# Kernel optimization log

Hardware: AMD Instinct MI355X
Metric: run time of the kernel (lower is better)

The kernel has to match this reference:

```python
import jax, jax.numpy as jnp
import numpy as np

B, S, DIM_IN = 2, 2048, 1024
H, DQ, DK = 16, 64, 64


def setup_inputs() -> dict:
    key = jax.random.key(0)
    ks = jax.random.split(key, 11)
    s_in = 1.0 / np.sqrt(DIM_IN)
    s_o = 1.0 / np.sqrt(H * DK)
    return {
        "Q": jax.random.normal(ks[0], (B, S, DIM_IN), jnp.float32),
        "K": jax.random.normal(ks[1], (B, S, DIM_IN), jnp.float32),
        "V": jax.random.normal(ks[2], (B, S, DIM_IN), jnp.float32),
        # per-head projection weights, stacked over heads: [H, dim_in, d]
        "Wq": jax.random.uniform(ks[3], (H, DIM_IN, DQ), jnp.float32, -s_in, s_in),
        "bq": jax.random.uniform(ks[4], (H, DQ), jnp.float32, -s_in, s_in),
        "Wk": jax.random.uniform(ks[5], (H, DIM_IN, DK), jnp.float32, -s_in, s_in),
        "bk": jax.random.uniform(ks[6], (H, DK), jnp.float32, -s_in, s_in),
        "Wv": jax.random.uniform(ks[7], (H, DIM_IN, DK), jnp.float32, -s_in, s_in),
        "bv": jax.random.uniform(ks[8], (H, DK), jnp.float32, -s_in, s_in),
        # output projection: Linear(H*DK, DIM_IN)
        "Wo": jax.random.uniform(ks[9], (H * DK, DIM_IN), jnp.float32, -s_o, s_o),
        "bo": jax.random.uniform(ks[10], (DIM_IN,), jnp.float32, -s_o, s_o),
    }


def reference(Q, K, V, Wq, bq, Wk, bk, Wv, bv, Wo, bo):
    # per-head linear projections: [B,S,din] x [H,din,d] -> [B,H,S,d]
    q = jnp.einsum("bsd,hdq->bhsq", Q, Wq) + bq[None, :, None, :]
    k = jnp.einsum("bsd,hdk->bhsk", K, Wk) + bk[None, :, None, :]
    v = jnp.einsum("bsd,hdk->bhsk", V, Wv) + bv[None, :, None, :]
    # scaled dot-product attention (full NxN scores, as in the original)
    scores = jnp.einsum("bhsq,bhtq->bhst", q, k) / jnp.sqrt(jnp.asarray(DQ, q.dtype))
    attn = jax.nn.softmax(scores, axis=-1)
    o = jnp.einsum("bhst,bhtk->bhsk", attn, v)  # [B,H,S,DK]
    # concat heads along feature dim, then output projection
    o = o.transpose(0, 2, 1, 3).reshape(Q.shape[0], Q.shape[1], -1)  # [B,S,H*DK]
    return o @ Wo + bo
```

## Files before the change

### kernel.cpp

```cpp
#include <hip/hip_runtime.h>
#include <hip/hip_bf16.h>

#define DIN 1024
#define NH 16
#define HD 64
#define SEQ 2048
#define NB 2

typedef __attribute__((ext_vector_type(8))) short bf16x8;
typedef __attribute__((ext_vector_type(4))) float f32x4;
typedef __attribute__((ext_vector_type(16))) float f32x16;

__device__ inline short f2bf(float f) {
  union { float f; unsigned u; } v; v.f = f;
  unsigned r = v.u + 0x7fff + ((v.u >> 16) & 1);
  return (short)(r >> 16);
}

__device__ inline unsigned pk2(float lo, float hi) {
  return (unsigned)(unsigned short)f2bf(lo) | ((unsigned)(unsigned short)f2bf(hi) << 16);
}

union U8 { unsigned u[4]; bf16x8 v; };
__device__ inline bf16x8 mkfrag(unsigned a, unsigned b, unsigned c, unsigned d) {
  U8 x; x.u[0] = a; x.u[1] = b; x.u[2] = c; x.u[3] = d; return x.v;
}

__device__ __forceinline__ void gload_lds16(const void* g, void* l) {
  __builtin_amdgcn_global_load_lds(
      (const __attribute__((address_space(1))) unsigned*)g,
      (__attribute__((address_space(3))) unsigned*)l, 16, 0, 0);
}

__global__ __launch_bounds__(256) void cvt_kernel(
    const float* __restrict__ Q, const float* __restrict__ K, const float* __restrict__ V,
    short* __restrict__ xq, short* __restrict__ xk, short* __restrict__ xv) {
  int z = blockIdx.y;
  const float* src = z == 0 ? Q : (z == 1 ? K : V);
  short* dst = z == 0 ? xq : (z == 1 ? xk : xv);
  size_t e = ((size_t)blockIdx.x * 256 + threadIdx.x) * 8;
  float4 x0 = *(const float4*)(src + e);
  float4 x1 = *(const float4*)(src + e + 4);
  bf16x8 v;
  v[0] = f2bf(x0.x); v[1] = f2bf(x0.y); v[2] = f2bf(x0.z); v[3] = f2bf(x0.w);
  v[4] = f2bf(x1.x); v[5] = f2bf(x1.y); v[6] = f2bf(x1.z); v[7] = f2bf(x1.w);
  *(bf16x8*)(dst + e) = v;
}

__global__ __launch_bounds__(256) void wt3_kernel(
    const float* __restrict__ Wq, const float* __restrict__ Wk, const float* __restrict__ Wv,
    short* __restrict__ out) {
  int zz = blockIdx.z; int which = zz >> 4, h = zz & 15;
  const float* in = (which == 0 ? Wq : (which == 1 ? Wk : Wv)) + (size_t)h * (DIN * HD);
  short* o = out + (size_t)which * (NH * HD * DIN) + (size_t)h * (HD * DIN);
  __shared__ float tile[64][65];
  int r0 = blockIdx.y * 64;
  int t = threadIdx.x;
  int r = t >> 2, cc = (t & 3) * 16;
#pragma unroll
  for (int j = 0; j < 16; ++j) tile[r][cc + j] = in[(size_t)(r0 + r) * HD + cc + j];
  __syncthreads();
  int c = t >> 2, rr = (t & 3) * 16;
#pragma unroll
  for (int j = 0; j < 16; ++j) o[(size_t)c * DIN + r0 + rr + j] = f2bf(tile[rr + j][c]);
}

__global__ __launch_bounds__(256) void wt_kernel(const float* __restrict__ in,
                                                 short* __restrict__ out, int R, int C) {
  __shared__ float tile[64][65];
  int r0 = blockIdx.y * 64, c0 = blockIdx.x * 64;
  int t = threadIdx.x;
  int r = t >> 2, cc = (t & 3) * 16;
#pragma unroll
  for (int j = 0; j < 16; ++j) tile[r][cc + j] = in[(size_t)(r0 + r) * C + c0 + cc + j];
  __syncthreads();
  int c = t >> 2, rr = (t & 3) * 16;
#pragma unroll
  for (int j = 0; j < 16; ++j) out[(size_t)(c0 + c) * R + r0 + rr + j] = f2bf(tile[rr + j][c]);
}

#define QSCL 0.18033688011112042f

__global__ __launch_bounds__(256) void proj_bf16_kernel(
    const short* __restrict__ xq, const short* __restrict__ xk, const short* __restrict__ xv,
    const short* __restrict__ wt,
    const float* __restrict__ bq, const float* __restrict__ bk, const float* __restrict__ bv,
    short* __restrict__ qb, short* __restrict__ kb, short* __restrict__ vt) {
  int mt = blockIdx.x, nt = blockIdx.y, z = blockIdx.z;
  const short* A = z == 0 ? xq : (z == 1 ? xk : xv);
  const short* Bt = wt + (size_t)z * (DIN * DIN);
  const float* bias = z == 0 ? bq : (z == 1 ? bk : bv);

  __shared__ __align__(16) short Al[128 * 32];
  __shared__ __align__(16) short Bl[128 * 32];

  int t = threadIdx.x, wid = t >> 6, lane = t & 63;
  int lrow = lane & 15, lhi = lane >> 4;
  int wr = wid >> 1, wc = wid & 1;
  int row0 = mt * 128, col0 = nt * 128;

  const short* aG = A + (size_t)(row0 + wid * 16 + (lane >> 2)) * DIN + (lane & 3) * 8;
  const short* bG = Bt + (size_t)(col0 + wid * 16 + (lane >> 2)) * DIN + (lane & 3) * 8;
  short* aL0 = &Al[wid * 512];
  short* aL1 = &Al[(4 + wid) * 512];
  short* bL0 = &Bl[wid * 512];
  short* bL1 = &Bl[(4 + wid) * 512];
  const short* aR = &Al[(wr * 64 + lrow) * 32 + lhi * 8];
  const short* bR = &Bl[(wc * 64 + lrow) * 32 + lhi * 8];

  f32x4 acc[4][4] = {};
  for (int kk = 0; kk < DIN; kk += 32) {
    gload_lds16(aG + kk, aL0);
    gload_lds16(aG + 64 * DIN + kk, aL1);
    gload_lds16(bG + kk, bL0);
    gload_lds16(bG + 64 * DIN + kk, bL1);
    __syncthreads();
    bf16x8 af[4], bfv[4];
#pragma unroll
    for (int m = 0; m < 4; ++m) af[m] = *(const bf16x8*)(aR + m * 512);
#pragma unroll
    for (int n = 0; n < 4; ++n) bfv[n] = *(const bf16x8*)(bR + n * 512);
#pragma unroll
    for (int m = 0; m < 4; ++m)
#pragma unroll
      for (int n = 0; n < 4; ++n)
        acc[m][n] = __builtin_amdgcn_mfma_f32_16x16x32_bf16(af[m], bfv[n], acc[m][n], 0, 0, 0);
    __syncthreads();
  }

#pragma unroll
  for (int m = 0; m < 4; ++m) {
#pragma unroll
    for (int n = 0; n < 4; ++n) {
      int c = col0 + wc * 64 + n * 16 + lrow;
      int h = c >> 6, hc = c & 63;
      float bval = bias[c];
#pragma unroll
      for (int i = 0; i < 4; ++i) {
        int r = row0 + wr * 64 + m * 16 + lhi * 4 + i;
        int b = r >> 11, s = r & 2047;
        float val = acc[m][n][i] + bval;
        if (z == 0) val *= QSCL;
        if (z == 2) vt[((size_t)(b * NH + h) * HD + hc) * SEQ + s] = f2bf(val);
        else {
          short* o = z == 0 ? qb : kb;
          o[((size_t)(b * NH + h) * SEQ + s) * HD + hc] = f2bf(val);
        }
      }
    }
  }
}

__global__ __launch_bounds__(256) void proj_f32_kernel(
    const float* __restrict__ Q, const float* __restrict__ K, const float* __restrict__ V,
    const short* __restrict__ wt,
    const float* __restrict__ bq, const float* __restrict__ bk, const float* __restrict__ bv,
    short* __restrict__ qb, short* __restrict__ kb, short* __restrict__ vt) {
  int mt = blockIdx.x, nt = blockIdx.y, z = blockIdx.z;
  const float* X = z == 0 ? Q : (z == 1 ? K : V);
  const short* Bt = wt + (size_t)z * (DIN * DIN);
  const float* bias = z == 0 ? bq : (z == 1 ? bk : bv);

  __shared__ __align__(16) short Al[128 * 32];
  __shared__ __align__(16) short Bl[128 * 32];

  int t = threadIdx.x, wid = t >> 6, lane = t & 63;
  int lrow = lane & 15, lhi = lane >> 4;
  int wr = wid >> 1, wc = wid & 1;
  int row0 = mt * 128, col0 = nt * 128;

  int arow = t >> 1, acol = (t & 1) * 16;
  const float* aF = X + (size_t)(row0 + arow) * DIN + acol;
  short* aW = &Al[arow * 32 + acol];

  const short* bG = Bt + (size_t)(col0 + wid * 16 + (lane >> 2)) * DIN + (lane & 3) * 8;
  short* bL0 = &Bl[wid * 512];
  short* bL1 = &Bl[(4 + wid) * 512];

  const short* aR = &Al[(wr * 64 + lrow) * 32 + lhi * 8];
  const short* bR = &Bl[(wc * 64 + lrow) * 32 + lhi * 8];

  f32x4 acc[4][4] = {};
  for (int kk = 0; kk < DIN; kk += 32) {
    gload_lds16(bG + kk, bL0);
    gload_lds16(bG + 64 * DIN + kk, bL1);
    float4 x0 = *(const float4*)(aF + kk);
    float4 x1 = *(const float4*)(aF + kk + 4);
    float4 x2 = *(const float4*)(aF + kk + 8);
    float4 x3 = *(const float4*)(aF + kk + 12);
    bf16x8 v0, v1;
    v0[0] = f2bf(x0.x); v0[1] = f2bf(x0.y); v0[2] = f2bf(x0.z); v0[3] = f2bf(x0.w);
    v0[4] = f2bf(x1.x); v0[5] = f2bf(x1.y); v0[6] = f2bf(x1.z); v0[7] = f2bf(x1.w);
    v1[0] = f2bf(x2.x); v1[1] = f2bf(x2.y); v1[2] = f2bf(x2.z); v1[3] = f2bf(x2.w);
    v1[4] = f2bf(x3.x); v1[5] = f2bf(x3.y); v1[6] = f2bf(x3.z); v1[7] = f2bf(x3.w);
    *(bf16x8*)aW = v0;
    *(bf16x8*)(aW + 8) = v1;
    __syncthreads();
    bf16x8 af[4], bfv[4];
#pragma unroll
    for (int m = 0; m < 4; ++m) af[m] = *(const bf16x8*)(aR + m * 512);
#pragma unroll
    for (int n = 0; n < 4; ++n) bfv[n] = *(const bf16x8*)(bR + n * 512);
#pragma unroll
    for (int m = 0; m < 4; ++m)
#pragma unroll
      for (int n = 0; n < 4; ++n)
        acc[m][n] = __builtin_amdgcn_mfma_f32_16x16x32_bf16(af[m], bfv[n], acc[m][n], 0, 0, 0);
    __syncthreads();
  }
#pragma unroll
  for (int m = 0; m < 4; ++m) {
#pragma unroll
    for (int n = 0; n < 4; ++n) {
      int c = col0 + wc * 64 + n * 16 + lrow;
      int h = c >> 6, hc = c & 63;
      float bval = bias[c];
#pragma unroll
      for (int i = 0; i < 4; ++i) {
        int r = row0 + wr * 64 + m * 16 + lhi * 4 + i;
        int b = r >> 11, s = r & 2047;
        float val = acc[m][n][i] + bval;
        if (z == 0) val *= QSCL;
        if (z == 2) vt[((size_t)(b * NH + h) * HD + hc) * SEQ + s] = f2bf(val);
        else {
          short* o = z == 0 ? qb : kb;
          o[((size_t)(b * NH + h) * SEQ + s) * HD + hc] = f2bf(val);
        }
      }
    }
  }
}

__global__ __launch_bounds__(256) void attn_kernel(
    const short* __restrict__ qb, const short* __restrict__ kb,
    const short* __restrict__ vt, short* __restrict__ ob) {
  int qt = blockIdx.x, h = blockIdx.y, bz = blockIdx.z;
  int t = threadIdx.x, wid = t >> 6, lane = t & 63;
  int l31 = lane & 31, hi = lane >> 5;

  __shared__ __align__(16) short kl[64 * 64];
  __shared__ __align__(16) short vl[64 * 64];

  size_t bh = (size_t)(bz * NH + h);
  const short* kbase = kb + bh * (size_t)SEQ * HD;
  const short* vbase = vt + bh * (size_t)HD * SEQ;

  int qg = qt * 128 + wid * 32 + l31;
  const short* qrow = qb + (bh * SEQ + qg) * HD + hi * 8;
  bf16x8 qf0 = *(const bf16x8*)(qrow);
  bf16x8 qf1 = *(const bf16x8*)(qrow + 16);
  bf16x8 qf2 = *(const bf16x8*)(qrow + 32);
  bf16x8 qf3 = *(const bf16x8*)(qrow + 48);

  int srow = wid * 16 + (lane >> 3);
  int swc = ((lane & 7) ^ (srow & 7)) * 8;
  const short* kg = kbase + (size_t)srow * HD + swc;
  const short* vg = vbase + (size_t)srow * SEQ + swc;
  short* klA = kl + wid * 1024; short* klB = klA + 512;
  short* vlA = vl + wid * 1024; short* vlB = vlA + 512;

  f32x16 o0, o1;
#pragma unroll
  for (int i = 0; i < 16; ++i) { o0[i] = 0.f; o1[i] = 0.f; }
  float mrun = -1e30f, lrun = 0.f;

  int ksw = (l31 & 7) << 3;

  for (int t0 = 0; t0 < SEQ; t0 += 64) {
    gload_lds16(kg + (size_t)t0 * HD, klA);
    gload_lds16(kg + (size_t)(t0 + 8) * HD, klB);
    gload_lds16(vg + t0, vlA);
    gload_lds16(vg + t0 + 8 * SEQ, vlB);
    __syncthreads();

    f32x16 c0, c1;
#pragma unroll
    for (int i = 0; i < 16; ++i) { c0[i] = 0.f; c1[i] = 0.f; }
#pragma unroll
    for (int dk = 0; dk < 4; ++dk) {
      int col = (dk * 16 + hi * 8) ^ ksw;
      bf16x8 ka = *(const bf16x8*)&kl[l31 * 64 + col];
      bf16x8 kc = *(const bf16x8*)&kl[(32 + l31) * 64 + col];
      bf16x8 qv = dk == 0 ? qf0 : dk == 1 ? qf1 : dk == 2 ? qf2 : qf3;
      c0 = __builtin_amdgcn_mfma_f32_32x32x16_bf16(ka, qv, c0, 0, 0, 0);
      c1 = __builtin_amdgcn_mfma_f32_32x32x16_bf16(kc, qv, c1, 0, 0, 0);
    }

    float mx = c0[0];
#pragma unroll
    for (int i = 1; i < 16; ++i) mx = fmaxf(mx, c0[i]);
#pragma unroll
    for (int i = 0; i < 16; ++i) mx = fmaxf(mx, c1[i]);
    mx = fmaxf(mx, __shfl_xor(mx, 32));
    if (!__all(mx - mrun <= 8.f)) {
      float mnew = fmaxf(mrun, mx);
      float corr = __builtin_amdgcn_exp2f(mrun - mnew);
      lrun *= corr;
#pragma unroll
      for (int i = 0; i < 16; ++i) { o0[i] *= corr; o1[i] *= corr; }
      mrun = mnew;
    }
#pragma unroll
    for (int i = 0; i < 16; ++i) c0[i] = __builtin_amdgcn_exp2f(c0[i] - mrun);
#pragma unroll
    for (int i = 0; i < 16; ++i) c1[i] = __builtin_amdgcn_exp2f(c1[i] - mrun);
    float ps = 0.f;
#pragma unroll
    for (int i = 0; i < 16; ++i) ps += c0[i];
#pragma unroll
    for (int i = 0; i < 16; ++i) ps += c1[i];
    ps += __shfl_xor(ps, 32);
    lrun += ps;

    unsigned u0 = pk2(c0[0], c0[1]),   u1 = pk2(c0[2], c0[3]);
    unsigned u2 = pk2(c0[4], c0[5]),   u3 = pk2(c0[6], c0[7]);
    unsigned u4 = pk2(c0[8], c0[9]),   u5 = pk2(c0[10], c0[11]);
    unsigned u6 = pk2(c0[12], c0[13]), u7 = pk2(c0[14], c0[15]);
    unsigned w0 = pk2(c1[0], c1[1]),   w1 = pk2(c1[2], c1[3]);
    unsigned w2 = pk2(c1[4], c1[5]),   w3 = pk2(c1[6], c1[7]);
    unsigned w4 = pk2(c1[8], c1[9]),   w5 = pk2(c1[10], c1[11]);
    unsigned w6 = pk2(c1[12], c1[13]), w7 = pk2(c1[14], c1[15]);
    unsigned x0 = __shfl_xor(u0, 32), x1 = __shfl_xor(u1, 32);
    unsigned x2 = __shfl_xor(u2, 32), x3 = __shfl_xor(u3, 32);
    unsigned x4 = __shfl_xor(u4, 32), x5 = __shfl_xor(u5, 32);
    unsigned x6 = __shfl_xor(u6, 32), x7 = __shfl_xor(u7, 32);
    unsigned y0 = __shfl_xor(w0, 32), y1 = __shfl_xor(w1, 32);
    unsigned y2 = __shfl_xor(w2, 32), y3 = __shfl_xor(w3, 32);
    unsigned y4 = __shfl_xor(w4, 32), y5 = __shfl_xor(w5, 32);
    unsigned y6 = __shfl_xor(w6, 32), y7 = __shfl_xor(w7, 32);
    bf16x8 fA0 = mkfrag(hi ? x2 : u0, hi ? x3 : u1, hi ? u2 : x0, hi ? u3 : x1);
    bf16x8 fA1 = mkfrag(hi ? x6 : u4, hi ? x7 : u5, hi ? u6 : x4, hi ? u7 : x5);
    bf16x8 fB0 = mkfrag(hi ? y2 : w0, hi ? y3 : w1, hi ? w2 : y0, hi ? w3 : y1);
    bf16x8 fB1 = mkfrag(hi ? y6 : w4, hi ? y7 : w5, hi ? w6 : y4, hi ? w7 : y5);

#pragma unroll
    for (int kc4 = 0; kc4 < 4; ++kc4) {
      bf16x8 pf = kc4 == 0 ? fA0 : kc4 == 1 ? fA1 : kc4 == 2 ? fB0 : fB1;
      int col = (kc4 * 16 + hi * 8) ^ ksw;
      bf16x8 va = *(const bf16x8*)&vl[l31 * 64 + col];
      bf16x8 vb = *(const bf16x8*)&vl[(32 + l31) * 64 + col];
      o0 = __builtin_amdgcn_mfma_f32_32x32x16_bf16(va, pf, o0, 0, 0, 0);
      o1 = __builtin_amdgcn_mfma_f32_32x32x16_bf16(vb, pf, o1, 0, 0, 0);
    }
    __syncthreads();
  }

  float inv = 1.0f / lrun;
  short* orow = ob + ((size_t)(bz * SEQ + qg)) * DIN + h * HD;
#pragma unroll
  for (int r = 0; r < 16; ++r) {
    int d = (r & 3) + 8 * (r >> 2) + 4 * hi;
    orow[d] = f2bf(o0[r] * inv);
    orow[32 + d] = f2bf(o1[r] * inv);
  }
}

__global__ __launch_bounds__(256) void oproj_kernel(
    const short* __restrict__ ob, const short* __restrict__ wto,
    const float* __restrict__ bo, float* __restrict__ out) {
  int mt = blockIdx.x, nt = blockIdx.y;
  __shared__ __align__(16) short Al[128 * 32];
  __shared__ __align__(16) short Bl[128 * 32];
  int t = threadIdx.x, wid = t >> 6, lane = t & 63;
  int lrow = lane & 15, lhi = lane >> 4;
  int wr = wid >> 1, wc = wid & 1;
  int row0 = mt * 128, col0 = nt * 128;

  const short* aG = ob + (size_t)(row0 + wid * 16 + (lane >> 2)) * DIN + (lane & 3) * 8;
  const short* bG = wto + (size_t)(col0 + wid * 16 + (lane >> 2)) * DIN + (lane & 3) * 8;
  short* aL0 = &Al[wid * 512];
  short* aL1 = &Al[(4 + wid) * 512];
  short* bL0 = &Bl[wid * 512];
  short* bL1 = &Bl[(4 + wid) * 512];
  const short* aR = &Al[(wr * 64 + lrow) * 32 + lhi * 8];
  const short* bR = &Bl[(wc * 64 + lrow) * 32 + lhi * 8];

  f32x4 acc[4][4] = {};
  for (int kk = 0; kk < DIN; kk += 32) {
    gload_lds16(aG + kk, aL0);
    gload_lds16(aG + 64 * DIN + kk, aL1);
    gload_lds16(bG + kk, bL0);
    gload_lds16(bG + 64 * DIN + kk, bL1);
    __syncthreads();
    bf16x8 af[4], bfv[4];
#pragma unroll
    for (int m = 0; m < 4; ++m) af[m] = *(const bf16x8*)(aR + m * 512);
#pragma unroll
    for (int n = 0; n < 4; ++n) bfv[n] = *(const bf16x8*)(bR + n * 512);
#pragma unroll
    for (int m = 0; m < 4; ++m)
#pragma unroll
      for (int n = 0; n < 4; ++n)
        acc[m][n] = __builtin_amdgcn_mfma_f32_16x16x32_bf16(af[m], bfv[n], acc[m][n], 0, 0, 0);
    __syncthreads();
  }
#pragma unroll
  for (int m = 0; m < 4; ++m) {
#pragma unroll
    for (int n = 0; n < 4; ++n) {
      int c = col0 + wc * 64 + n * 16 + lrow;
      float bval = bo[c];
#pragma unroll
      for (int i = 0; i < 4; ++i) {
        int r = row0 + wr * 64 + m * 16 + lhi * 4 + i;
        out[(size_t)r * DIN + c] = acc[m][n][i] + bval;
      }
    }
  }
}

extern "C" void kernel_launch(void* const* d_in, const int* in_sizes, int n_in,
                              void* d_out, int out_size, void* d_ws, size_t ws_size,
                              hipStream_t stream) {
  const float* Q  = (const float*)d_in[0];
  const float* K  = (const float*)d_in[1];
  const float* V  = (const float*)d_in[2];
  const float* Wq = (const float*)d_in[3];
  const float* bq = (const float*)d_in[4];
  const float* Wk = (const float*)d_in[5];
  const float* bk = (const float*)d_in[6];
  const float* Wv = (const float*)d_in[7];
  const float* bv = (const float*)d_in[8];
  const float* Wo = (const float*)d_in[9];
  const float* bo = (const float*)d_in[10];
  float* out = (float*)d_out;

  short* ws = (short*)d_ws;
  const size_t NX = (size_t)NB * SEQ * DIN;
  const size_t NW = (size_t)NH * HD * DIN;
  short* qbuf = ws;
  short* kbuf = qbuf + NX;
  short* vtb  = kbuf + NX;
  short* obuf = vtb + NX;
  short* wtq  = obuf + NX;
  short* wto  = wtq + 3 * NW;
  short* xq = wto + NW;
  short* xk = xq + NX;
  short* xv = xk + NX;
  const size_t need_big = (7 * NX + 4 * NW) * sizeof(short);

  wt3_kernel<<<dim3(1, 16, 48), 256, 0, stream>>>(Wq, Wk, Wv, wtq);
  wt_kernel<<<dim3(16, 16, 1), 256, 0, stream>>>(Wo, wto, DIN, DIN);
  if (ws_size >= need_big) {
    cvt_kernel<<<dim3(2048, 3), 256, 0, stream>>>(Q, K, V, xq, xk, xv);
    proj_bf16_kernel<<<dim3(32, 8, 3), 256, 0, stream>>>(xq, xk, xv, wtq, bq, bk, bv,
                                                         qbuf, kbuf, vtb);
  } else {
    proj_f32_kernel<<<dim3(32, 8, 3), 256, 0, stream>>>(Q, K, V, wtq, bq, bk, bv,
                                                        qbuf, kbuf, vtb);
  }
  attn_kernel<<<dim3(16, 16, 2), 256, 0, stream>>>(qbuf, kbuf, vtb, obuf);
  oproj_kernel<<<dim3(32, 8), 256, 0, stream>>>(obuf, wto, bo, out);
}
```

Measured before the change: 250.0 us.

## Double-buffer attention K/V tiles, tree reductions, hw bf16 pack, smaller oproj tiles

The attention kernel now double-buffers its K/V tiles in LDS, issuing the next tile's async global-to-LDS loads before computing on the current one. This is meant to hide load latency behind the MFMAs. Row max and sum reductions become tree reductions to shorten dependency chains, and the float-to-bf16 pack uses the v_cvt_pk_bf16_f32 instruction instead of software rounding. The output projection tile shrinks from 128 to 64 rows, doubling the grid to raise occupancy and CU coverage, at the cost of more B-operand reloads and double the LDS in attention.

```diff
diff --git a/kernel.cpp b/kernel.cpp
--- a/kernel.cpp
+++ b/kernel.cpp
@@ -18,7 +18,9 @@
 }
 
 __device__ inline unsigned pk2(float lo, float hi) {
-  return (unsigned)(unsigned short)f2bf(lo) | ((unsigned)(unsigned short)f2bf(hi) << 16);
+  unsigned r;
+  asm("v_cvt_pk_bf16_f32 %0, %1, %2" : "=v"(r) : "v"(lo), "v"(hi));
+  return r;
 }
 
 union U8 { unsigned u[4]; bf16x8 v; };
@@ -238,8 +240,8 @@
   int t = threadIdx.x, wid = t >> 6, lane = t & 63;
   int l31 = lane & 31, hi = lane >> 5;
 
-  __shared__ __align__(16) short kl[64 * 64];
-  __shared__ __align__(16) short vl[64 * 64];
+  __shared__ __align__(16) short kl[2][64 * 64];
+  __shared__ __align__(16) short vl[2][64 * 64];
 
   size_t bh = (size_t)(bz * NH + h);
   const short* kbase = kb + bh * (size_t)SEQ * HD;
@@ -256,8 +258,6 @@
   int swc = ((lane & 7) ^ (srow & 7)) * 8;
   const short* kg = kbase + (size_t)srow * HD + swc;
   const short* vg = vbase + (size_t)srow * SEQ + swc;
-  short* klA = kl + wid * 1024; short* klB = klA + 512;
-  short* vlA = vl + wid * 1024; short* vlB = vlA + 512;
 
   f32x16 o0, o1;
 #pragma unroll
@@ -266,12 +266,20 @@
 
   int ksw = (l31 & 7) << 3;
 
+#define STAGE(T0, B)                                                   \
+  do {                                                                 \
+    gload_lds16(kg + (size_t)(T0)*HD, &kl[B][wid * 1024]);             \
+    gload_lds16(kg + (size_t)((T0) + 8) * HD, &kl[B][wid * 1024 + 512]); \
+    gload_lds16(vg + (T0), &vl[B][wid * 1024]);                        \
+    gload_lds16(vg + (T0) + 8 * SEQ, &vl[B][wid * 1024 + 512]);        \
+  } while (0)
+
+  STAGE(0, 0);
+  __syncthreads();
+  int cur = 0;
+
   for (int t0 = 0; t0 < SEQ; t0 += 64) {
-    gload_lds16(kg + (size_t)t0 * HD, klA);
-    gload_lds16(kg + (size_t)(t0 + 8) * HD, klB);
-    gload_lds16(vg + t0, vlA);
-    gload_lds16(vg + t0 + 8 * SEQ, vlB);
-    __syncthreads();
+    if (t0 + 64 < SEQ) STAGE(t0 + 64, cur ^ 1);
 
     f32x16 c0, c1;
 #pragma unroll
@@ -279,18 +287,21 @@
 #pragma unroll
     for (int dk = 0; dk < 4; ++dk) {
       int col = (dk * 16 + hi * 8) ^ ksw;
-      bf16x8 ka = *(const bf16x8*)&kl[l31 * 64 + col];
-      bf16x8 kc = *(const bf16x8*)&kl[(32 + l31) * 64 + col];
+      bf16x8 ka = *(const bf16x8*)&kl[cur][l31 * 64 + col];
+      bf16x8 kc = *(const bf16x8*)&kl[cur][(32 + l31) * 64 + col];
       bf16x8 qv = dk == 0 ? qf0 : dk == 1 ? qf1 : dk == 2 ? qf2 : qf3;
       c0 = __builtin_amdgcn_mfma_f32_32x32x16_bf16(ka, qv, c0, 0, 0, 0);
       c1 = __builtin_amdgcn_mfma_f32_32x32x16_bf16(kc, qv, c1, 0, 0, 0);
     }
 
-    float mx = c0[0];
-#pragma unroll
-    for (int i = 1; i < 16; ++i) mx = fmaxf(mx, c0[i]);
-#pragma unroll
-    for (int i = 0; i < 16; ++i) mx = fmaxf(mx, c1[i]);
+    float tm[16];
+#pragma unroll
+    for (int i = 0; i < 16; ++i) tm[i] = fmaxf(c0[i], c1[i]);
+#pragma unroll
+    for (int i = 0; i < 8; ++i) tm[i] = fmaxf(tm[i], tm[i + 8]);
+#pragma unroll
+    for (int i = 0; i < 4; ++i) tm[i] = fmaxf(tm[i], tm[i + 4]);
+    float mx = fmaxf(fmaxf(tm[0], tm[1]), fmaxf(tm[2], tm[3]));
     mx = fmaxf(mx, __shfl_xor(mx, 32));
     if (!__all(mx - mrun <= 8.f)) {
       float mnew = fmaxf(mrun, mx);
@@ -304,11 +315,14 @@
     for (int i = 0; i < 16; ++i) c0[i] = __builtin_amdgcn_exp2f(c0[i] - mrun);
 #pragma unroll
     for (int i = 0; i < 16; ++i) c1[i] = __builtin_amdgcn_exp2f(c1[i] - mrun);
-    float ps = 0.f;
-#pragma unroll
-    for (int i = 0; i < 16; ++i) ps += c0[i];
-#pragma unroll
-    for (int i = 0; i < 16; ++i) ps += c1[i];
+    float ts[16];
+#pragma unroll
+    for (int i = 0; i < 16; ++i) ts[i] = c0[i] + c1[i];
+#pragma unroll
+    for (int i = 0; i < 8; ++i) ts[i] += ts[i + 8];
+#pragma unroll
+    for (int i = 0; i < 4; ++i) ts[i] += ts[i + 4];
+    float ps = (ts[0] + ts[1]) + (ts[2] + ts[3]);
     ps += __shfl_xor(ps, 32);
     lrun += ps;
 
@@ -337,13 +351,15 @@
     for (int kc4 = 0; kc4 < 4; ++kc4) {
       bf16x8 pf = kc4 == 0 ? fA0 : kc4 == 1 ? fA1 : kc4 == 2 ? fB0 : fB1;
       int col = (kc4 * 16 + hi * 8) ^ ksw;
-      bf16x8 va = *(const bf16x8*)&vl[l31 * 64 + col];
-      bf16x8 vb = *(const bf16x8*)&vl[(32 + l31) * 64 + col];
+      bf16x8 va = *(const bf16x8*)&vl[cur][l31 * 64 + col];
+      bf16x8 vb = *(const bf16x8*)&vl[cur][(32 + l31) * 64 + col];
       o0 = __builtin_amdgcn_mfma_f32_32x32x16_bf16(va, pf, o0, 0, 0, 0);
       o1 = __builtin_amdgcn_mfma_f32_32x32x16_bf16(vb, pf, o1, 0, 0, 0);
     }
     __syncthreads();
-  }
+    cur ^= 1;
+  }
+#undef STAGE
 
   float inv = 1.0f / lrun;
   short* orow = ob + ((size_t)(bz * SEQ + qg)) * DIN + h * HD;
@@ -359,50 +375,48 @@
     const short* __restrict__ ob, const short* __restrict__ wto,
     const float* __restrict__ bo, float* __restrict__ out) {
   int mt = blockIdx.x, nt = blockIdx.y;
-  __shared__ __align__(16) short Al[128 * 32];
+  __shared__ __align__(16) short Al[64 * 32];
   __shared__ __align__(16) short Bl[128 * 32];
   int t = threadIdx.x, wid = t >> 6, lane = t & 63;
   int lrow = lane & 15, lhi = lane >> 4;
   int wr = wid >> 1, wc = wid & 1;
-  int row0 = mt * 128, col0 = nt * 128;
+  int row0 = mt * 64, col0 = nt * 128;
 
   const short* aG = ob + (size_t)(row0 + wid * 16 + (lane >> 2)) * DIN + (lane & 3) * 8;
   const short* bG = wto + (size_t)(col0 + wid * 16 + (lane >> 2)) * DIN + (lane & 3) * 8;
-  short* aL0 = &Al[wid * 512];
-  short* aL1 = &Al[(4 + wid) * 512];
+  short* aL = &Al[wid * 512];
   short* bL0 = &Bl[wid * 512];
   short* bL1 = &Bl[(4 + wid) * 512];
-  const short* aR = &Al[(wr * 64 + lrow) * 32 + lhi * 8];
+  const short* aR = &Al[(wr * 32 + lrow) * 32 + lhi * 8];
   const short* bR = &Bl[(wc * 64 + lrow) * 32 + lhi * 8];
 
-  f32x4 acc[4][4] = {};
+  f32x4 acc[2][4] = {};
   for (int kk = 0; kk < DIN; kk += 32) {
-    gload_lds16(aG + kk, aL0);
-    gload_lds16(aG + 64 * DIN + kk, aL1);
+    gload_lds16(aG + kk, aL);
     gload_lds16(bG + kk, bL0);
     gload_lds16(bG + 64 * DIN + kk, bL1);
     __syncthreads();
-    bf16x8 af[4], bfv[4];
-#pragma unroll
-    for (int m = 0; m < 4; ++m) af[m] = *(const bf16x8*)(aR + m * 512);
+    bf16x8 af[2], bfv[4];
+#pragma unroll
+    for (int m = 0; m < 2; ++m) af[m] = *(const bf16x8*)(aR + m * 512);
 #pragma unroll
     for (int n = 0; n < 4; ++n) bfv[n] = *(const bf16x8*)(bR + n * 512);
 #pragma unroll
-    for (int m = 0; m < 4; ++m)
+    for (int m = 0; m < 2; ++m)
 #pragma unroll
       for (int n = 0; n < 4; ++n)
         acc[m][n] = __builtin_amdgcn_mfma_f32_16x16x32_bf16(af[m], bfv[n], acc[m][n], 0, 0, 0);
     __syncthreads();
   }
 #pragma unroll
-  for (int m = 0; m < 4; ++m) {
+  for (int m = 0; m < 2; ++m) {
 #pragma unroll
     for (int n = 0; n < 4; ++n) {
       int c = col0 + wc * 64 + n * 16 + lrow;
       float bval = bo[c];
 #pragma unroll
       for (int i = 0; i < 4; ++i) {
-        int r = row0 + wr * 64 + m * 16 + lhi * 4 + i;
+        int r = row0 + wr * 32 + m * 16 + lhi * 4 + i;
         out[(size_t)r * DIN + c] = acc[m][n][i] + bval;
       }
     }
@@ -450,5 +464,5 @@
                                                         qbuf, kbuf, vtb);
   }
   attn_kernel<<<dim3(16, 16, 2), 256, 0, stream>>>(qbuf, kbuf, vtb, obuf);
-  oproj_kernel<<<dim3(32, 8), 256, 0, stream>>>(obuf, wto, bo, out);
-}
+  oproj_kernel<<<dim3(64, 8), 256, 0, stream>>>(obuf, wto, bo, out);
+}
```

Measured after the change: 245.4 us. About the same (-1.8%).
